# Kernel optimization log

Hardware: AMD Instinct MI355X
Metric: run time of the kernel (lower is better)

The kernel has to match this reference:

```python
import jax, jax.numpy as jnp
import numpy as np

NEG_SLOPE = 0.2
EPS = 1e-16


def glorot(key, shape):
    fan = shape[0] + shape[-1] if len(shape) == 2 else shape[-1] * 2
    lim = jnp.sqrt(6.0 / fan)
    return jax.random.uniform(key, shape, minval=-lim, maxval=lim, dtype=jnp.float32)


def setup_inputs() -> dict:
    key = jax.random.key(0)
    ks = jax.random.split(key, 16)
    B, N, E = 4, 50000, 800000
    F_in, H, C, n_cls = 128, 4, 16, 16
    x = jax.random.normal(ks[0], (B, N, F_in), dtype=jnp.float32)
    edge_index = jax.random.randint(ks[1], (2, E), 0, N, dtype=jnp.int64)
    inp = {
        "x": x,
        "edge_index": edge_index,
        # layer 1: 128 -> 4 heads x 16, concat
        "W1": glorot(ks[2], (F_in, H * C)),
        "a1s": glorot(ks[3], (H, C)),
        "a1d": glorot(ks[4], (H, C)),
        "b1": jnp.zeros((H * C,), jnp.float32),
        # layer 2: 64 -> 4 heads x 16, concat
        "W2": glorot(ks[5], (H * C, H * C)),
        "a2s": glorot(ks[6], (H, C)),
        "a2d": glorot(ks[7], (H, C)),
        "b2": jnp.zeros((H * C,), jnp.float32),
        # layer 3: 64 -> 1 head x num_classes, concat
        "W3": glorot(ks[8], (H * C, n_cls)),
        "a3s": glorot(ks[9], (1, n_cls)),
        "a3d": glorot(ks[10], (1, n_cls)),
        "b3": jnp.zeros((n_cls,), jnp.float32),
    }
    return inp


def gat_conv(x, W, a_src, a_dst, b, src, dst, N, concat):
    # x: [N, F_in]; W: [F_in, H*C]
    H, C = a_src.shape
    h = (x @ W).reshape(N, H, C)
    e_src = jnp.einsum('nhc,hc->nh', h, a_src)  # [N, H]
    e_dst = jnp.einsum('nhc,hc->nh', h, a_dst)  # [N, H]
    e = jax.nn.leaky_relu(e_src[src] + e_dst[dst], NEG_SLOPE)  # [E, H]
    # segment softmax over incoming edges of each target node
    m = jax.ops.segment_max(e, dst, num_segments=N)  # [N, H]
    ex = jnp.exp(e - m[dst])
    denom = jax.ops.segment_sum(ex, dst, num_segments=N)  # [N, H]
    alpha = ex / (denom[dst] + EPS)  # [E, H]
    out = jax.ops.segment_sum(alpha[:, :, None] * h[src], dst, num_segments=N)  # [N, H, C]
    out = out.reshape(N, H * C) if concat else out.mean(axis=1)
    return out + b


def reference(x, edge_index, W1, a1s, a1d, b1, W2, a2s, a2d, b2, W3, a3s, a3d, b3):
    B, N, _ = x.shape
    # add self-loops (PyG GATConv default)
    loop = jnp.arange(N, dtype=edge_index.dtype)
    src = jnp.concatenate([edge_index[0], loop])
    dst = jnp.concatenate([edge_index[1], loop])

    def fwd_single(xi):
        h = jax.nn.relu(gat_conv(xi, W1, a1s, a1d, b1, src, dst, N, True))
        h = jax.nn.relu(gat_conv(h, W2, a2s, a2d, b2, src, dst, N, True))
        return gat_conv(h, W3, a3s, a3d, b3, src, dst, N, True)

    return jax.vmap(fwd_single)(x)  # [B, N, num_classes]
```

## Files before the change

### kernel.cpp

```cpp
#include <hip/hip_runtime.h>
#include <hip/hip_bf16.h>
#include <hip/hip_fp16.h>
#include <math.h>


#define NEG_SLOPE 0.2f

constexpr int NN   = 50000;
constexpr int FIN  = 128;
constexpr int HC   = 64;
constexpr int NCLS = 16;

struct H16 { __half2 h[8]; };
struct H4  { __half2 h[2]; };


__global__ void init_deg_kernel(int* deg, int N) {
    int t = blockIdx.x * blockDim.x + threadIdx.x;
    if (t < N) deg[t] = 1;
}

__global__ void hist_kernel(const int* __restrict__ ei, int* deg, int E) {
    int t = blockIdx.x * blockDim.x + threadIdx.x;
    if (t < E) atomicAdd(&deg[ei[E + t]], 1);
}

__global__ __launch_bounds__(1024) void scan1_kernel(
    const int* __restrict__ deg, int* __restrict__ rp,
    int* __restrict__ bsum, int N) {
    __shared__ int buf[1024];
    int i = blockIdx.x * 1024 + threadIdx.x;
    int v = (i < N) ? deg[i] : 0;
    buf[threadIdx.x] = v;
    __syncthreads();
#pragma unroll
    for (int off = 1; off < 1024; off <<= 1) {
        int t = (threadIdx.x >= (unsigned)off) ? buf[threadIdx.x - off] : 0;
        __syncthreads();
        buf[threadIdx.x] += t;
        __syncthreads();
    }
    if (i < N) rp[i] = buf[threadIdx.x] - v;
    if (threadIdx.x == 1023) bsum[blockIdx.x] = buf[1023];
}

__global__ void scan2_kernel(int* __restrict__ bsum, int nb,
                             int* __restrict__ rp, int N) {
    int lane = threadIdx.x;
    int v = (lane < nb) ? bsum[lane] : 0;
#pragma unroll
    for (int off = 1; off < 64; off <<= 1) {
        int t = __shfl_up(v, off);
        if (lane >= off) v += t;
    }
    if (lane < nb) bsum[lane] = v;
    if (lane == nb - 1) rp[N] = v;
}

__global__ __launch_bounds__(1024) void scan3_kernel(
    int* __restrict__ rp, int* __restrict__ wp,
    const int* __restrict__ bsum, int N) {
    int i = blockIdx.x * 1024 + threadIdx.x;
    if (i >= N) return;
    int add = (blockIdx.x > 0) ? bsum[blockIdx.x - 1] : 0;
    int r = rp[i] + add;
    rp[i] = r;
    wp[i] = r;
}

__global__ void scatter_kernel(const int* __restrict__ ei, int* wp,
                               int* __restrict__ col, int E, int N) {
    int t = blockIdx.x * blockDim.x + threadIdx.x;
    int total = E + N;
    if (t >= total) return;
    if (t < E) {
        int s = ei[t];
        int d = ei[E + t];
        int pos = atomicAdd(&wp[d], 1);
        col[pos] = s;
    } else {
        int n = t - E;
        int pos = atomicAdd(&wp[n], 1);
        col[pos] = n;
    }
}


template <int K, int M, int RN, int BF, bool IL>
__global__ __launch_bounds__(256) void gemm_kernel(
    const float* __restrict__ X, const float* __restrict__ W,
    const float* __restrict__ as_, const float* __restrict__ ad_,
    __half* __restrict__ Hout, float* __restrict__ Es, float* __restrict__ Ed,
    int N) {
    constexpr int G  = M / 4;
    constexpr int NG = 256 / G;
    constexpr int NT = NG * RN;
    constexpr int H  = M / 16;
    __shared__ float Ws[K * M];
    const int b = blockIdx.y;
    const int t = threadIdx.x;
    for (int i = t; i < K * M / 4; i += 256)
        reinterpret_cast<float4*>(Ws)[i] = reinterpret_cast<const float4*>(W)[i];
    __syncthreads();

    const int cg = t % G;
    const int ng = t / G;
    const int c0 = cg * 4;
    const int node0 = blockIdx.x * NT + ng * RN;

    const float* xp[RN];
#pragma unroll
    for (int j = 0; j < RN; ++j) {
        int node = node0 + j;
        int nc = (node < N) ? node : 0;
        xp[j] = X + (IL ? ((size_t)nc * BF + b) * (size_t)K
                        : ((size_t)b * N + nc) * (size_t)K);
    }

    float acc[RN][4];
#pragma unroll
    for (int j = 0; j < RN; ++j)
#pragma unroll
        for (int cc = 0; cc < 4; ++cc) acc[j][cc] = 0.f;

#pragma unroll 4
    for (int k = 0; k < K; k += 4) {
        float4 w0 = *reinterpret_cast<const float4*>(&Ws[(k + 0) * M + c0]);
        float4 w1 = *reinterpret_cast<const float4*>(&Ws[(k + 1) * M + c0]);
        float4 w2 = *reinterpret_cast<const float4*>(&Ws[(k + 2) * M + c0]);
        float4 w3 = *reinterpret_cast<const float4*>(&Ws[(k + 3) * M + c0]);
#pragma unroll
        for (int j = 0; j < RN; ++j) {
            float4 xv = *reinterpret_cast<const float4*>(&xp[j][k]);
            acc[j][0] = fmaf(xv.x, w0.x, acc[j][0]);
            acc[j][1] = fmaf(xv.x, w0.y, acc[j][1]);
            acc[j][2] = fmaf(xv.x, w0.z, acc[j][2]);
            acc[j][3] = fmaf(xv.x, w0.w, acc[j][3]);
            acc[j][0] = fmaf(xv.y, w1.x, acc[j][0]);
            acc[j][1] = fmaf(xv.y, w1.y, acc[j][1]);
            acc[j][2] = fmaf(xv.y, w1.z, acc[j][2]);
            acc[j][3] = fmaf(xv.y, w1.w, acc[j][3]);
            acc[j][0] = fmaf(xv.z, w2.x, acc[j][0]);
            acc[j][1] = fmaf(xv.z, w2.y, acc[j][1]);
            acc[j][2] = fmaf(xv.z, w2.z, acc[j][2]);
            acc[j][3] = fmaf(xv.z, w2.w, acc[j][3]);
            acc[j][0] = fmaf(xv.w, w3.x, acc[j][0]);
            acc[j][1] = fmaf(xv.w, w3.y, acc[j][1]);
            acc[j][2] = fmaf(xv.w, w3.z, acc[j][2]);
            acc[j][3] = fmaf(xv.w, w3.w, acc[j][3]);
        }
    }

    const int hd = c0 >> 4;
    const float4 av = *reinterpret_cast<const float4*>(&as_[c0]);
    const float4 dv = *reinterpret_cast<const float4*>(&ad_[c0]);
#pragma unroll
    for (int j = 0; j < RN; ++j) {
        int node = node0 + j;
        float ps = acc[j][0] * av.x + acc[j][1] * av.y +
                   acc[j][2] * av.z + acc[j][3] * av.w;
        float pd = acc[j][0] * dv.x + acc[j][1] * dv.y +
                   acc[j][2] * dv.z + acc[j][3] * dv.w;
        ps += __shfl_xor(ps, 1); ps += __shfl_xor(ps, 2);
        pd += __shfl_xor(pd, 1); pd += __shfl_xor(pd, 2);
        if (node < N) {
            H4 hv;
            hv.h[0] = __float22half2_rn(make_float2(acc[j][0], acc[j][1]));
            hv.h[1] = __float22half2_rn(make_float2(acc[j][2], acc[j][3]));
            *reinterpret_cast<H4*>(&Hout[((size_t)node * BF + b) * M + c0]) = hv;
            if ((cg & 3) == 0) {
                Es[((size_t)node * BF + b) * H + hd] = ps;
                Ed[((size_t)node * BF + b) * H + hd] = pd;
            }
        }
    }
}


template <int H, bool RELU, bool OUTB, int BF>
__global__ __launch_bounds__(256) void agg_kernel(
    const int* __restrict__ rp, const int* __restrict__ col,
    const __half* __restrict__ Hm, const float* __restrict__ Es,
    const float* __restrict__ Ed, const float* __restrict__ bias,
    float* __restrict__ Out, int N) {
    constexpr int C = 16;
    constexpr int M = H * C;
    int t = blockIdx.x * 256 + threadIdx.x;
    if (t >= N * H * BF) return;
    int u = t;
    const int b  = u % BF; u /= BF;
    const int hd = u % H;  u /= H;
    const int n  = u;

    const float ed = Ed[((size_t)n * BF + b) * H + hd];
    const int beg = rp[n], end = rp[n + 1];

    float m = -1e30f, dn = 0.f;
    float acc[C];
#pragma unroll
    for (int j = 0; j < C; ++j) acc[j] = 0.f;

    int i = beg;
    int sA = col[i];
    float esA = Es[((size_t)sA * BF + b) * H + hd];
    H16 hA = *reinterpret_cast<const H16*>(Hm + ((size_t)sA * BF + b) * M + hd * C);

    while (true) {
        int inext = i + 1;
        bool more = (inext < end);
        int sB = 0; float esB = 0.f; H16 hB;
        if (more) {
            sB = col[inext];
            esB = Es[((size_t)sB * BF + b) * H + hd];
            hB = *reinterpret_cast<const H16*>(Hm + ((size_t)sB * BF + b) * M + hd * C);
        }

        float e = esA + ed;
        e = (e >= 0.f) ? e : NEG_SLOPE * e;
        float2 f0 = __half22float2(hA.h[0]);
        float2 f1 = __half22float2(hA.h[1]);
        float2 f2 = __half22float2(hA.h[2]);
        float2 f3 = __half22float2(hA.h[3]);
        float2 f4 = __half22float2(hA.h[4]);
        float2 f5 = __half22float2(hA.h[5]);
        float2 f6 = __half22float2(hA.h[6]);
        float2 f7 = __half22float2(hA.h[7]);
        if (e > m) {
            float sc = __expf(m - e);
            m = e;
            dn = fmaf(dn, sc, 1.0f);
            acc[0]=fmaf(acc[0],sc,f0.x);   acc[1]=fmaf(acc[1],sc,f0.y);
            acc[2]=fmaf(acc[2],sc,f1.x);   acc[3]=fmaf(acc[3],sc,f1.y);
            acc[4]=fmaf(acc[4],sc,f2.x);   acc[5]=fmaf(acc[5],sc,f2.y);
            acc[6]=fmaf(acc[6],sc,f3.x);   acc[7]=fmaf(acc[7],sc,f3.y);
            acc[8]=fmaf(acc[8],sc,f4.x);   acc[9]=fmaf(acc[9],sc,f4.y);
            acc[10]=fmaf(acc[10],sc,f5.x); acc[11]=fmaf(acc[11],sc,f5.y);
            acc[12]=fmaf(acc[12],sc,f6.x); acc[13]=fmaf(acc[13],sc,f6.y);
            acc[14]=fmaf(acc[14],sc,f7.x); acc[15]=fmaf(acc[15],sc,f7.y);
        } else {
            float ex = __expf(e - m);
            dn += ex;
            acc[0]=fmaf(ex,f0.x,acc[0]);   acc[1]=fmaf(ex,f0.y,acc[1]);
            acc[2]=fmaf(ex,f1.x,acc[2]);   acc[3]=fmaf(ex,f1.y,acc[3]);
            acc[4]=fmaf(ex,f2.x,acc[4]);   acc[5]=fmaf(ex,f2.y,acc[5]);
            acc[6]=fmaf(ex,f3.x,acc[6]);   acc[7]=fmaf(ex,f3.y,acc[7]);
            acc[8]=fmaf(ex,f4.x,acc[8]);   acc[9]=fmaf(ex,f4.y,acc[9]);
            acc[10]=fmaf(ex,f5.x,acc[10]); acc[11]=fmaf(ex,f5.y,acc[11]);
            acc[12]=fmaf(ex,f6.x,acc[12]); acc[13]=fmaf(ex,f6.y,acc[13]);
            acc[14]=fmaf(ex,f7.x,acc[14]); acc[15]=fmaf(ex,f7.y,acc[15]);
        }
        if (!more) break;
        i = inext; sA = sB; esA = esB; hA = hB;
    }

    float inv = 1.f / (dn + 1e-16f);
    const float* bp = bias + hd * C;
    float* op = OUTB ? (Out + ((size_t)b * N + n) * M + hd * C)
                     : (Out + ((size_t)n * BF + b) * M + hd * C);
    float vb[C];
#pragma unroll
    for (int j = 0; j < C; ++j) {
        float v = fmaf(acc[j], inv, bp[j]);
        if (RELU) v = fmaxf(v, 0.f);
        vb[j] = v;
    }
    *reinterpret_cast<float4*>(op + 0)  = make_float4(vb[0], vb[1], vb[2], vb[3]);
    *reinterpret_cast<float4*>(op + 4)  = make_float4(vb[4], vb[5], vb[6], vb[7]);
    *reinterpret_cast<float4*>(op + 8)  = make_float4(vb[8], vb[9], vb[10], vb[11]);
    *reinterpret_cast<float4*>(op + 12) = make_float4(vb[12], vb[13], vb[14], vb[15]);
}


extern "C" void kernel_launch(void* const* d_in, const int* in_sizes, int n_in,
                              void* d_out, int out_size, void* d_ws, size_t ws_size,
                              hipStream_t stream) {
    const float* x   = (const float*)d_in[0];
    const int*   ei  = (const int*)d_in[1];
    const float* W1  = (const float*)d_in[2];
    const float* a1s = (const float*)d_in[3];
    const float* a1d = (const float*)d_in[4];
    const float* b1  = (const float*)d_in[5];
    const float* W2  = (const float*)d_in[6];
    const float* a2s = (const float*)d_in[7];
    const float* a2d = (const float*)d_in[8];
    const float* b2  = (const float*)d_in[9];
    const float* W3  = (const float*)d_in[10];
    const float* a3s = (const float*)d_in[11];
    const float* a3d = (const float*)d_in[12];
    const float* b3  = (const float*)d_in[13];
    float* outp = (float*)d_out;

    const int N  = NN;
    const int E  = in_sizes[1] / 2;
    const int ET = E + N;
    const int B  = in_sizes[0] / (N * FIN);
    const int NB1024 = (N + 1023) / 1024;

    char* ws = (char*)d_ws;
    size_t off = 0;
    auto alloc = [&](size_t bytes) -> void* {
        void* p = ws + off;
        off += (bytes + 255) & ~(size_t)255;
        return p;
    };
    int* deg  = (int*)alloc((size_t)N * 4);
    int* rp   = (int*)alloc((size_t)(N + 1) * 4);
    int* wp   = (int*)alloc((size_t)N * 4);
    int* bsum = (int*)alloc(64 * 4);
    int* col  = (int*)alloc((size_t)ET * 4);

    size_t fused_need = off + ((size_t)N * B * HC * 2 + 256)
                            + ((size_t)N * B * HC * 4 + 256)
                            + 2 * ((size_t)N * B * 4 * 4 + 256);
    bool fused = (B == 4) && (ws_size >= fused_need);
    int BF = fused ? 4 : 1;

    __half* h  = (__half*)alloc((size_t)N * BF * HC * 2);
    float* z   = (float*)alloc((size_t)N * BF * HC * 4);
    float* es  = (float*)alloc((size_t)N * BF * 4 * 4);
    float* edv = (float*)alloc((size_t)N * BF * 4 * 4);

    init_deg_kernel<<<(N + 255) / 256, 256, 0, stream>>>(deg, N);
    hist_kernel<<<(E + 255) / 256, 256, 0, stream>>>(ei, deg, E);
    scan1_kernel<<<NB1024, 1024, 0, stream>>>(deg, rp, bsum, N);
    scan2_kernel<<<1, 64, 0, stream>>>(bsum, NB1024, rp, N);
    scan3_kernel<<<NB1024, 1024, 0, stream>>>(rp, wp, bsum, N);
    scatter_kernel<<<(ET + 255) / 256, 256, 0, stream>>>(ei, wp, col, E, N);

    if (fused) {
        dim3 g12((N + 63) / 64, 4);
        dim3 g3((N + 127) / 128, 4);
        int agg12 = (N * 4 * 4 + 255) / 256;
        int agg3  = (N * 4 + 255) / 256;
        gemm_kernel<128, 64, 4, 4, false><<<g12, 256, 0, stream>>>(x, W1, a1s, a1d, h, es, edv, N);
        agg_kernel<4, true, false, 4><<<agg12, 256, 0, stream>>>(rp, col, h, es, edv, b1, z, N);
        gemm_kernel<64, 64, 4, 4, true><<<g12, 256, 0, stream>>>(z, W2, a2s, a2d, h, es, edv, N);
        agg_kernel<4, true, false, 4><<<agg12, 256, 0, stream>>>(rp, col, h, es, edv, b2, z, N);
        gemm_kernel<64, 16, 2, 4, true><<<g3, 256, 0, stream>>>(z, W3, a3s, a3d, h, es, edv, N);
        agg_kernel<1, false, true, 4><<<agg3, 256, 0, stream>>>(rp, col, h, es, edv, b3, outp, N);
    } else {
        dim3 g12((N + 63) / 64, 1);
        dim3 g3((N + 127) / 128, 1);
        int agg12 = (N * 4 + 255) / 256;
        int agg3  = (N + 255) / 256;
        for (int b = 0; b < B; ++b) {
            const float* xb = x + (size_t)b * N * FIN;
            float* outb = outp + (size_t)b * N * NCLS;
            gemm_kernel<128, 64, 4, 1, false><<<g12, 256, 0, stream>>>(xb, W1, a1s, a1d, h, es, edv, N);
            agg_kernel<4, true, false, 1><<<agg12, 256, 0, stream>>>(rp, col, h, es, edv, b1, z, N);
            gemm_kernel<64, 64, 4, 1, false><<<g12, 256, 0, stream>>>(z, W2, a2s, a2d, h, es, edv, N);
            agg_kernel<4, true, false, 1><<<agg12, 256, 0, stream>>>(rp, col, h, es, edv, b2, z, N);
            gemm_kernel<64, 16, 2, 1, false><<<g3, 256, 0, stream>>>(z, W3, a3s, a3d, h, es, edv, N);
            agg_kernel<1, false, false, 1><<<agg3, 256, 0, stream>>>(rp, col, h, es, edv, b3, outb, N);
        }
    }
}
```

Baseline: 580.0 us.

## Stage node feature tiles in shared memory and read weights from global

The dense projection kernel now loads each block's node-feature rows into padded LDS with coalesced float4 loads, where before it staged the weight matrix in LDS and had each thread stream its rows directly from global memory. Weights are now read straight from global memory and rely on the cache, since every thread reads the same small matrix. The third-layer GEMM is re-tiled to one row per thread, with its grid resized to match. The aim is better coalescing of the large activation reads, paid for with per-iteration global weight loads and a different LDS footprint.

```diff
diff --git a/kernel.cpp b/kernel.cpp
--- a/kernel.cpp
+++ b/kernel.cpp
@@ -92,30 +92,32 @@
     const float* __restrict__ as_, const float* __restrict__ ad_,
     __half* __restrict__ Hout, float* __restrict__ Es, float* __restrict__ Ed,
     int N) {
-    constexpr int G  = M / 4;
-    constexpr int NG = 256 / G;
-    constexpr int NT = NG * RN;
-    constexpr int H  = M / 16;
-    __shared__ float Ws[K * M];
+    constexpr int G   = M / 4;
+    constexpr int NG  = 256 / G;
+    constexpr int NT  = NG * RN;
+    constexpr int H   = M / 16;
+    constexpr int LK  = K + 4;
+    __shared__ float xs[NT * LK];
     const int b = blockIdx.y;
     const int t = threadIdx.x;
-    for (int i = t; i < K * M / 4; i += 256)
-        reinterpret_cast<float4*>(Ws)[i] = reinterpret_cast<const float4*>(W)[i];
+    const int node00 = blockIdx.x * NT;
+
+    for (int idx = t * 4; idx < NT * K; idx += 1024) {
+        int row = idx / K;
+        int k   = idx & (K - 1);
+        int node = node00 + row;
+        int nc = (node < N) ? node : N - 1;
+        const float* src = X + (IL ? ((size_t)nc * BF + b) * (size_t)K
+                                   : ((size_t)b * N + nc) * (size_t)K) + k;
+        *reinterpret_cast<float4*>(&xs[row * LK + k]) =
+            *reinterpret_cast<const float4*>(src);
+    }
     __syncthreads();
 
     const int cg = t % G;
     const int ng = t / G;
     const int c0 = cg * 4;
-    const int node0 = blockIdx.x * NT + ng * RN;
-
-    const float* xp[RN];
-#pragma unroll
-    for (int j = 0; j < RN; ++j) {
-        int node = node0 + j;
-        int nc = (node < N) ? node : 0;
-        xp[j] = X + (IL ? ((size_t)nc * BF + b) * (size_t)K
-                        : ((size_t)b * N + nc) * (size_t)K);
-    }
+    const int node0 = node00 + ng * RN;
 
     float acc[RN][4];
 #pragma unroll
@@ -123,15 +125,16 @@
 #pragma unroll
         for (int cc = 0; cc < 4; ++cc) acc[j][cc] = 0.f;
 
-#pragma unroll 4
+#pragma unroll 2
     for (int k = 0; k < K; k += 4) {
-        float4 w0 = *reinterpret_cast<const float4*>(&Ws[(k + 0) * M + c0]);
-        float4 w1 = *reinterpret_cast<const float4*>(&Ws[(k + 1) * M + c0]);
-        float4 w2 = *reinterpret_cast<const float4*>(&Ws[(k + 2) * M + c0]);
-        float4 w3 = *reinterpret_cast<const float4*>(&Ws[(k + 3) * M + c0]);
+        float4 w0 = *reinterpret_cast<const float4*>(&W[(k + 0) * M + c0]);
+        float4 w1 = *reinterpret_cast<const float4*>(&W[(k + 1) * M + c0]);
+        float4 w2 = *reinterpret_cast<const float4*>(&W[(k + 2) * M + c0]);
+        float4 w3 = *reinterpret_cast<const float4*>(&W[(k + 3) * M + c0]);
 #pragma unroll
         for (int j = 0; j < RN; ++j) {
-            float4 xv = *reinterpret_cast<const float4*>(&xp[j][k]);
+            float4 xv = *reinterpret_cast<const float4*>(
+                &xs[(ng * RN + j) * LK + k]);
             acc[j][0] = fmaf(xv.x, w0.x, acc[j][0]);
             acc[j][1] = fmaf(xv.x, w0.y, acc[j][1]);
             acc[j][2] = fmaf(xv.x, w0.z, acc[j][2]);
@@ -329,18 +332,18 @@
 
     if (fused) {
         dim3 g12((N + 63) / 64, 4);
-        dim3 g3((N + 127) / 128, 4);
+        dim3 g3((N + 63) / 64, 4);
         int agg12 = (N * 4 * 4 + 255) / 256;
         int agg3  = (N * 4 + 255) / 256;
         gemm_kernel<128, 64, 4, 4, false><<<g12, 256, 0, stream>>>(x, W1, a1s, a1d, h, es, edv, N);
         agg_kernel<4, true, false, 4><<<agg12, 256, 0, stream>>>(rp, col, h, es, edv, b1, z, N);
         gemm_kernel<64, 64, 4, 4, true><<<g12, 256, 0, stream>>>(z, W2, a2s, a2d, h, es, edv, N);
         agg_kernel<4, true, false, 4><<<agg12, 256, 0, stream>>>(rp, col, h, es, edv, b2, z, N);
-        gemm_kernel<64, 16, 2, 4, true><<<g3, 256, 0, stream>>>(z, W3, a3s, a3d, h, es, edv, N);
+        gemm_kernel<64, 16, 1, 4, true><<<g3, 256, 0, stream>>>(z, W3, a3s, a3d, h, es, edv, N);
         agg_kernel<1, false, true, 4><<<agg3, 256, 0, stream>>>(rp, col, h, es, edv, b3, outp, N);
     } else {
         dim3 g12((N + 63) / 64, 1);
-        dim3 g3((N + 127) / 128, 1);
+        dim3 g3((N + 63) / 64, 1);
         int agg12 = (N * 4 + 255) / 256;
         int agg3  = (N + 255) / 256;
         for (int b = 0; b < B; ++b) {
@@ -350,7 +353,7 @@
             agg_kernel<4, true, false, 1><<<agg12, 256, 0, stream>>>(rp, col, h, es, edv, b1, z, N);
             gemm_kernel<64, 64, 4, 1, false><<<g12, 256, 0, stream>>>(z, W2, a2s, a2d, h, es, edv, N);
             agg_kernel<4, true, false, 1><<<agg12, 256, 0, stream>>>(rp, col, h, es, edv, b2, z, N);
-            gemm_kernel<64, 16, 2, 1, false><<<g3, 256, 0, stream>>>(z, W3, a3s, a3d, h, es, edv, N);
+            gemm_kernel<64, 16, 1, 1, false><<<g3, 256, 0, stream>>>(z, W3, a3s, a3d, h, es, edv, N);
             agg_kernel<1, false, false, 1><<<agg3, 256, 0, stream>>>(rp, col, h, es, edv, b3, outb, N);
         }
     }
```

Result: slower. 594.9 us (+2.6%).

## Use fp16 MFMA for dense projections and store hidden activations in fp16

Applied to the files above, without the earlier changes.

Replaces the scalar FP32 FMA GEMM with a kernel that stages X and a pre-transposed fp16 weight copy in shared memory and computes with 16x16x16 f16 MFMA instructions. The attention dot products are reduced with wave shuffles. The aggregation kernel now writes intermediate layer outputs as fp16, halving the bytes read and written between layers. This lowers GEMM compute and memory traffic but quantizes inputs and intermediates to fp16, which adds rounding error.

```diff
diff --git a/kernel.cpp b/kernel.cpp
--- a/kernel.cpp
+++ b/kernel.cpp
@@ -11,8 +11,10 @@
 constexpr int HC   = 64;
 constexpr int NCLS = 16;
 
+typedef _Float16 half4 __attribute__((ext_vector_type(4)));
+typedef float    f32x4 __attribute__((ext_vector_type(4)));
+
 struct H16 { __half2 h[8]; };
-struct H4  { __half2 h[2]; };
 
 
 __global__ void init_deg_kernel(int* deg, int N) {
@@ -86,103 +88,126 @@
 }
 
 
-template <int K, int M, int RN, int BF, bool IL>
-__global__ __launch_bounds__(256) void gemm_kernel(
-    const float* __restrict__ X, const float* __restrict__ W,
+__global__ void prep_w_kernel(const float* __restrict__ W1,
+                              const float* __restrict__ W2,
+                              const float* __restrict__ W3,
+                              __half* __restrict__ Wt1,
+                              __half* __restrict__ Wt2,
+                              __half* __restrict__ Wt3) {
+    int t = blockIdx.x * 256 + threadIdx.x;
+    if (t < 64 * 128) { int c = t >> 7, k = t & 127; Wt1[t] = __float2half(W1[k * 64 + c]); }
+    if (t < 64 * 64)  { int c = t >> 6, k = t & 63;  Wt2[t] = __float2half(W2[k * 64 + c]); }
+    if (t < 16 * 64)  { int c = t >> 6, k = t & 63;  Wt3[t] = __float2half(W3[k * 16 + c]); }
+}
+
+
+template <int K, int M, int BF, bool IN16>
+__global__ __launch_bounds__(256) void gemm_mfma_kernel(
+    const void* __restrict__ Xin, const __half* __restrict__ Wt_g,
     const float* __restrict__ as_, const float* __restrict__ ad_,
     __half* __restrict__ Hout, float* __restrict__ Es, float* __restrict__ Ed,
     int N) {
-    constexpr int G  = M / 4;
-    constexpr int NG = 256 / G;
-    constexpr int NT = NG * RN;
-    constexpr int H  = M / 16;
-    __shared__ float Ws[K * M];
+    constexpr int CT = M / 16;
+    constexpr int PK = K + 8;
+    constexpr int KS = K / 16;
+    __shared__ _Float16 Xs[64 * PK];
+    __shared__ _Float16 Ws[M * PK];
     const int b = blockIdx.y;
     const int t = threadIdx.x;
-    for (int i = t; i < K * M / 4; i += 256)
-        reinterpret_cast<float4*>(Ws)[i] = reinterpret_cast<const float4*>(W)[i];
+    const int node00 = blockIdx.x * 64;
+
+    {
+        const float4* wsrc = reinterpret_cast<const float4*>(Wt_g);
+        constexpr int WC8 = K / 8;
+        for (int idx = t; idx < M * WC8; idx += 256) {
+            int c = idx / WC8, kk = idx - c * WC8;
+            *reinterpret_cast<float4*>(&Ws[c * PK + kk * 8]) = wsrc[idx];
+        }
+    }
+    if (IN16) {
+        const __half* Xh = (const __half*)Xin;
+        constexpr int C8 = K / 8;
+        for (int idx = t; idx < 64 * C8; idx += 256) {
+            int row = idx / C8, k8 = idx - row * C8;
+            int node = node00 + row;
+            if (node >= N) node = N - 1;
+            const float4* src = reinterpret_cast<const float4*>(
+                Xh + ((size_t)node * BF + b) * K + k8 * 8);
+            *reinterpret_cast<float4*>(&Xs[row * PK + k8 * 8]) = *src;
+        }
+    } else {
+        const float* Xf = (const float*)Xin;
+        constexpr int C4 = K / 4;
+        for (int idx = t; idx < 64 * C4; idx += 256) {
+            int row = idx / C4, k4 = idx - row * C4;
+            int node = node00 + row;
+            if (node >= N) node = N - 1;
+            float4 xv = *reinterpret_cast<const float4*>(
+                Xf + ((size_t)b * N + node) * K + k4 * 4);
+            half4 hv;
+            hv[0] = (_Float16)xv.x; hv[1] = (_Float16)xv.y;
+            hv[2] = (_Float16)xv.z; hv[3] = (_Float16)xv.w;
+            *reinterpret_cast<half4*>(&Xs[row * PK + k4 * 4]) = hv;
+        }
+    }
     __syncthreads();
 
-    const int cg = t % G;
-    const int ng = t / G;
-    const int c0 = cg * 4;
-    const int node0 = blockIdx.x * NT + ng * RN;
-
-    const float* xp[RN];
-#pragma unroll
-    for (int j = 0; j < RN; ++j) {
-        int node = node0 + j;
-        int nc = (node < N) ? node : 0;
-        xp[j] = X + (IL ? ((size_t)nc * BF + b) * (size_t)K
-                        : ((size_t)b * N + nc) * (size_t)K);
-    }
-
-    float acc[RN][4];
-#pragma unroll
-    for (int j = 0; j < RN; ++j)
-#pragma unroll
-        for (int cc = 0; cc < 4; ++cc) acc[j][cc] = 0.f;
-
-#pragma unroll 4
-    for (int k = 0; k < K; k += 4) {
-        float4 w0 = *reinterpret_cast<const float4*>(&Ws[(k + 0) * M + c0]);
-        float4 w1 = *reinterpret_cast<const float4*>(&Ws[(k + 1) * M + c0]);
-        float4 w2 = *reinterpret_cast<const float4*>(&Ws[(k + 2) * M + c0]);
-        float4 w3 = *reinterpret_cast<const float4*>(&Ws[(k + 3) * M + c0]);
-#pragma unroll
-        for (int j = 0; j < RN; ++j) {
-            float4 xv = *reinterpret_cast<const float4*>(&xp[j][k]);
-            acc[j][0] = fmaf(xv.x, w0.x, acc[j][0]);
-            acc[j][1] = fmaf(xv.x, w0.y, acc[j][1]);
-            acc[j][2] = fmaf(xv.x, w0.z, acc[j][2]);
-            acc[j][3] = fmaf(xv.x, w0.w, acc[j][3]);
-            acc[j][0] = fmaf(xv.y, w1.x, acc[j][0]);
-            acc[j][1] = fmaf(xv.y, w1.y, acc[j][1]);
-            acc[j][2] = fmaf(xv.y, w1.z, acc[j][2]);
-            acc[j][3] = fmaf(xv.y, w1.w, acc[j][3]);
-            acc[j][0] = fmaf(xv.z, w2.x, acc[j][0]);
-            acc[j][1] = fmaf(xv.z, w2.y, acc[j][1]);
-            acc[j][2] = fmaf(xv.z, w2.z, acc[j][2]);
-            acc[j][3] = fmaf(xv.z, w2.w, acc[j][3]);
-            acc[j][0] = fmaf(xv.w, w3.x, acc[j][0]);
-            acc[j][1] = fmaf(xv.w, w3.y, acc[j][1]);
-            acc[j][2] = fmaf(xv.w, w3.z, acc[j][2]);
-            acc[j][3] = fmaf(xv.w, w3.w, acc[j][3]);
-        }
-    }
-
-    const int hd = c0 >> 4;
-    const float4 av = *reinterpret_cast<const float4*>(&as_[c0]);
-    const float4 dv = *reinterpret_cast<const float4*>(&ad_[c0]);
-#pragma unroll
-    for (int j = 0; j < RN; ++j) {
-        int node = node0 + j;
-        float ps = acc[j][0] * av.x + acc[j][1] * av.y +
-                   acc[j][2] * av.z + acc[j][3] * av.w;
-        float pd = acc[j][0] * dv.x + acc[j][1] * dv.y +
-                   acc[j][2] * dv.z + acc[j][3] * dv.w;
-        ps += __shfl_xor(ps, 1); ps += __shfl_xor(ps, 2);
-        pd += __shfl_xor(pd, 1); pd += __shfl_xor(pd, 2);
-        if (node < N) {
-            H4 hv;
-            hv.h[0] = __float22half2_rn(make_float2(acc[j][0], acc[j][1]));
-            hv.h[1] = __float22half2_rn(make_float2(acc[j][2], acc[j][3]));
-            *reinterpret_cast<H4*>(&Hout[((size_t)node * BF + b) * M + c0]) = hv;
-            if ((cg & 3) == 0) {
-                Es[((size_t)node * BF + b) * H + hd] = ps;
-                Ed[((size_t)node * BF + b) * H + hd] = pd;
+    const int lane = t & 63;
+    const int w    = t >> 6;
+    const int l15  = lane & 15;
+    const int lg   = lane >> 4;
+    const int rowb = w * 16;
+
+    f32x4 acc[CT];
+#pragma unroll
+    for (int ct = 0; ct < CT; ++ct)
+#pragma unroll
+        for (int r = 0; r < 4; ++r) acc[ct][r] = 0.f;
+
+#pragma unroll
+    for (int ks = 0; ks < KS; ++ks) {
+        half4 a = *reinterpret_cast<const half4*>(
+            &Xs[(rowb + l15) * PK + ks * 16 + lg * 4]);
+#pragma unroll
+        for (int ct = 0; ct < CT; ++ct) {
+            half4 bf = *reinterpret_cast<const half4*>(
+                &Ws[(ct * 16 + l15) * PK + ks * 16 + lg * 4]);
+            acc[ct] = __builtin_amdgcn_mfma_f32_16x16x16f16(a, bf, acc[ct], 0, 0, 0);
+        }
+    }
+
+    _Float16* Hh = reinterpret_cast<_Float16*>(Hout);
+#pragma unroll
+    for (int ct = 0; ct < CT; ++ct) {
+        float a_s = as_[ct * 16 + l15];
+        float a_d = ad_[ct * 16 + l15];
+#pragma unroll
+        for (int r = 0; r < 4; ++r) {
+            int node = node00 + rowb + lg * 4 + r;
+            float hv = acc[ct][r];
+            float ps = hv * a_s, pd = hv * a_d;
+            ps += __shfl_xor(ps, 1); ps += __shfl_xor(ps, 2);
+            ps += __shfl_xor(ps, 4); ps += __shfl_xor(ps, 8);
+            pd += __shfl_xor(pd, 1); pd += __shfl_xor(pd, 2);
+            pd += __shfl_xor(pd, 4); pd += __shfl_xor(pd, 8);
+            if (node < N) {
+                Hh[((size_t)node * BF + b) * M + ct * 16 + l15] = (_Float16)hv;
+                if (l15 == 0) {
+                    Es[((size_t)node * BF + b) * CT + ct] = ps;
+                    Ed[((size_t)node * BF + b) * CT + ct] = pd;
+                }
             }
         }
     }
 }
 
 
-template <int H, bool RELU, bool OUTB, int BF>
+template <int H, bool RELU, bool OUTB, bool OUTH, int BF>
 __global__ __launch_bounds__(256) void agg_kernel(
     const int* __restrict__ rp, const int* __restrict__ col,
     const __half* __restrict__ Hm, const float* __restrict__ Es,
     const float* __restrict__ Ed, const float* __restrict__ bias,
-    float* __restrict__ Out, int N) {
+    void* __restrict__ Out, int N) {
     constexpr int C = 16;
     constexpr int M = H * C;
     int t = blockIdx.x * 256 + threadIdx.x;
@@ -255,8 +280,6 @@
 
     float inv = 1.f / (dn + 1e-16f);
     const float* bp = bias + hd * C;
-    float* op = OUTB ? (Out + ((size_t)b * N + n) * M + hd * C)
-                     : (Out + ((size_t)n * BF + b) * M + hd * C);
     float vb[C];
 #pragma unroll
     for (int j = 0; j < C; ++j) {
@@ -264,10 +287,21 @@
         if (RELU) v = fmaxf(v, 0.f);
         vb[j] = v;
     }
-    *reinterpret_cast<float4*>(op + 0)  = make_float4(vb[0], vb[1], vb[2], vb[3]);
-    *reinterpret_cast<float4*>(op + 4)  = make_float4(vb[4], vb[5], vb[6], vb[7]);
-    *reinterpret_cast<float4*>(op + 8)  = make_float4(vb[8], vb[9], vb[10], vb[11]);
-    *reinterpret_cast<float4*>(op + 12) = make_float4(vb[12], vb[13], vb[14], vb[15]);
+    if (OUTH) {
+        __half* op = (__half*)Out + ((size_t)n * BF + b) * M + hd * C;
+        H16 hv;
+#pragma unroll
+        for (int j = 0; j < 8; ++j)
+            hv.h[j] = __float22half2_rn(make_float2(vb[2 * j], vb[2 * j + 1]));
+        *reinterpret_cast<H16*>(op) = hv;
+    } else {
+        float* op = OUTB ? ((float*)Out + ((size_t)b * N + n) * M + hd * C)
+                         : ((float*)Out + ((size_t)n * BF + b) * M + hd * C);
+        *reinterpret_cast<float4*>(op + 0)  = make_float4(vb[0], vb[1], vb[2], vb[3]);
+        *reinterpret_cast<float4*>(op + 4)  = make_float4(vb[4], vb[5], vb[6], vb[7]);
+        *reinterpret_cast<float4*>(op + 8)  = make_float4(vb[8], vb[9], vb[10], vb[11]);
+        *reinterpret_cast<float4*>(op + 12) = make_float4(vb[12], vb[13], vb[14], vb[15]);
+    }
 }
 
 
@@ -308,15 +342,17 @@
     int* wp   = (int*)alloc((size_t)N * 4);
     int* bsum = (int*)alloc(64 * 4);
     int* col  = (int*)alloc((size_t)ET * 4);
-
-    size_t fused_need = off + ((size_t)N * B * HC * 2 + 256)
-                            + ((size_t)N * B * HC * 4 + 256)
+    __half* Wt1 = (__half*)alloc(64 * 128 * 2);
+    __half* Wt2 = (__half*)alloc(64 * 64 * 2);
+    __half* Wt3 = (__half*)alloc(16 * 64 * 2);
+
+    size_t fused_need = off + 2 * ((size_t)N * B * HC * 2 + 256)
                             + 2 * ((size_t)N * B * 4 * 4 + 256);
     bool fused = (B == 4) && (ws_size >= fused_need);
     int BF = fused ? 4 : 1;
 
     __half* h  = (__half*)alloc((size_t)N * BF * HC * 2);
-    float* z   = (float*)alloc((size_t)N * BF * HC * 4);
+    __half* z  = (__half*)alloc((size_t)N * BF * HC * 2);
     float* es  = (float*)alloc((size_t)N * BF * 4 * 4);
     float* edv = (float*)alloc((size_t)N * BF * 4 * 4);
 
@@ -326,32 +362,31 @@
     scan2_kernel<<<1, 64, 0, stream>>>(bsum, NB1024, rp, N);
     scan3_kernel<<<NB1024, 1024, 0, stream>>>(rp, wp, bsum, N);
     scatter_kernel<<<(ET + 255) / 256, 256, 0, stream>>>(ei, wp, col, E, N);
+    prep_w_kernel<<<32, 256, 0, stream>>>(W1, W2, W3, Wt1, Wt2, Wt3);
 
     if (fused) {
-        dim3 g12((N + 63) / 64, 4);
-        dim3 g3((N + 127) / 128, 4);
+        dim3 g((N + 63) / 64, 4);
         int agg12 = (N * 4 * 4 + 255) / 256;
         int agg3  = (N * 4 + 255) / 256;
-        gemm_kernel<128, 64, 4, 4, false><<<g12, 256, 0, stream>>>(x, W1, a1s, a1d, h, es, edv, N);
-        agg_kernel<4, true, false, 4><<<agg12, 256, 0, stream>>>(rp, col, h, es, edv, b1, z, N);
-        gemm_kernel<64, 64, 4, 4, true><<<g12, 256, 0, stream>>>(z, W2, a2s, a2d, h, es, edv, N);
-        agg_kernel<4, true, false, 4><<<agg12, 256, 0, stream>>>(rp, col, h, es, edv, b2, z, N);
-        gemm_kernel<64, 16, 2, 4, true><<<g3, 256, 0, stream>>>(z, W3, a3s, a3d, h, es, edv, N);
-        agg_kernel<1, false, true, 4><<<agg3, 256, 0, stream>>>(rp, col, h, es, edv, b3, outp, N);
+        gemm_mfma_kernel<128, 64, 4, false><<<g, 256, 0, stream>>>(x, Wt1, a1s, a1d, h, es, edv, N);
+        agg_kernel<4, true, false, true, 4><<<agg12, 256, 0, stream>>>(rp, col, h, es, edv, b1, z, N);
+        gemm_mfma_kernel<64, 64, 4, true><<<g, 256, 0, stream>>>(z, Wt2, a2s, a2d, h, es, edv, N);
+        agg_kernel<4, true, false, true, 4><<<agg12, 256, 0, stream>>>(rp, col, h, es, edv, b2, z, N);
+        gemm_mfma_kernel<64, 16, 4, true><<<g, 256, 0, stream>>>(z, Wt3, a3s, a3d, h, es, edv, N);
+        agg_kernel<1, false, true, false, 4><<<agg3, 256, 0, stream>>>(rp, col, h, es, edv, b3, outp, N);
     } else {
-        dim3 g12((N + 63) / 64, 1);
-        dim3 g3((N + 127) / 128, 1);
+        dim3 g((N + 63) / 64, 1);
         int agg12 = (N * 4 + 255) / 256;
         int agg3  = (N + 255) / 256;
         for (int b = 0; b < B; ++b) {
             const float* xb = x + (size_t)b * N * FIN;
             float* outb = outp + (size_t)b * N * NCLS;
-            gemm_kernel<128, 64, 4, 1, false><<<g12, 256, 0, stream>>>(xb, W1, a1s, a1d, h, es, edv, N);
-            agg_kernel<4, true, false, 1><<<agg12, 256, 0, stream>>>(rp, col, h, es, edv, b1, z, N);
-            gemm_kernel<64, 64, 4, 1, false><<<g12, 256, 0, stream>>>(z, W2, a2s, a2d, h, es, edv, N);
-            agg_kernel<4, true, false, 1><<<agg12, 256, 0, stream>>>(rp, col, h, es, edv, b2, z, N);
-            gemm_kernel<64, 16, 2, 1, false><<<g3, 256, 0, stream>>>(z, W3, a3s, a3d, h, es, edv, N);
-            agg_kernel<1, false, false, 1><<<agg3, 256, 0, stream>>>(rp, col, h, es, edv, b3, outb, N);
-        }
-    }
-}
+            gemm_mfma_kernel<128, 64, 1, false><<<g, 256, 0, stream>>>(xb, Wt1, a1s, a1d, h, es, edv, N);
+            agg_kernel<4, true, false, true, 1><<<agg12, 256, 0, stream>>>(rp, col, h, es, edv, b1, z, N);
+            gemm_mfma_kernel<64, 64, 1, true><<<g, 256, 0, stream>>>(z, Wt2, a2s, a2d, h, es, edv, N);
+            agg_kernel<4, true, false, true, 1><<<agg12, 256, 0, stream>>>(rp, col, h, es, edv, b2, z, N);
+            gemm_mfma_kernel<64, 16, 1, true><<<g, 256, 0, stream>>>(z, Wt3, a3s, a3d, h, es, edv, N);
+            agg_kernel<1, false, false, false, 1><<<agg3, 256, 0, stream>>>(rp, col, h, es, edv, b3, outb, N);
+        }
+    }
+}
```

Result: faster. 542.1 us (-6.5%).
